# Optimization experiments

Measured on AMD Instinct MI355X. Metric: run time of the kernel, lower is better.

Reference implementation:

```python
import jax, jax.numpy as jnp
import numpy as np
import math

B, S, D, H_HEADS, K_SPAN = 2, 2048, 64, 12, 512  # batch, seq, head dim, heads, pos_ebd_size


def setup_inputs() -> dict:
    key = jax.random.key(0)
    ks = jax.random.split(key, 12)
    init = lambda k, shp: (jax.random.normal(k, shp, dtype=jnp.float32) * 0.02)
    H = jax.random.normal(ks[0], (B, S, D), dtype=jnp.float32)
    pos_embeddings = jax.random.normal(ks[1], (2 * K_SPAN, D), dtype=jnp.float32)
    # classic DeBERTa relative positions: i - j (2-D, as required by the torch code path)
    idx = jnp.arange(S)
    relative_pos = (idx[:, None] - idx[None, :]).astype(jnp.int64)
    OH = H_HEADS * D
    return {
        "H": H,
        "pos_embeddings": pos_embeddings,
        "relative_pos": relative_pos,
        "Wq": init(ks[2], (OH, D)), "bq": jnp.zeros((OH,), jnp.float32),
        "Wk": init(ks[3], (OH, D)), "bk": jnp.zeros((OH,), jnp.float32),
        "Wv": init(ks[4], (OH, D)), "bv": jnp.zeros((OH,), jnp.float32),
        "Wpq": init(ks[5], (OH, D)), "bpq": jnp.zeros((OH,), jnp.float32),
        "Wpk": init(ks[6], (OH, D)), "bpk": jnp.zeros((OH,), jnp.float32),
    }


def _heads(x):
    # [..., S, h*d] -> [..., h, S, d]
    b, s, _ = x.shape
    return x.reshape(b, s, H_HEADS, D).transpose(0, 2, 1, 3)


def reference(H, pos_embeddings, relative_pos, Wq, bq, Wk, bk, Wv, bv, Wpq, bpq, Wpk, bpk):
    proj = lambda x, W, b: x @ W.T + b
    q = _heads(proj(H, Wq, bq))  # [B,h,S,d]
    k = _heads(proj(H, Wk, bk))
    v = _heads(proj(H, Wv, bv))

    # content-to-content scores
    scores = jnp.einsum('bhqd,bhkd->bhqk', q, k)  # [B,h,S,S]

    # relative position projections over the full 2K span
    pk = proj(pos_embeddings, Wpk, bpk).reshape(2 * K_SPAN, H_HEADS, D).transpose(1, 0, 2)  # [h,2K,d]
    pq = proj(pos_embeddings, Wpq, bpq).reshape(2 * K_SPAN, H_HEADS, D).transpose(1, 0, 2)

    rel = relative_pos.astype(jnp.int32)
    # content-to-position: gather over 2K axis with clamped (i-j)+K
    c2p = jnp.einsum('bhqd,hrd->bhqr', q, pk)  # [B,h,S,2K]
    c2p_pos = jnp.clip(rel + K_SPAN, 0, 2 * K_SPAN - 1)  # [S,S]
    c2p_idx = jnp.broadcast_to(c2p_pos[None, None], (B, H_HEADS, S, S))
    c2p_att = jnp.take_along_axis(c2p, c2p_idx, axis=-1)  # [B,h,S,S]

    # position-to-content: gather over 2K axis with clamped -(i-j)+K, then transpose
    p2c = jnp.einsum('bhkd,hrd->bhkr', k, pq)  # [B,h,S,2K]
    p2c_pos = jnp.clip(-rel + K_SPAN, 0, 2 * K_SPAN - 1)
    p2c_idx = jnp.broadcast_to(p2c_pos[None, None], (B, H_HEADS, S, S))
    p2c_att = jnp.take_along_axis(p2c, p2c_idx, axis=-1).swapaxes(-1, -2)  # [B,h,S,S]

    scores = (scores + c2p_att + p2c_att) / math.sqrt(D * 3)
    probs = jax.nn.softmax(scores, axis=-1)
    ctx = jnp.einsum('bhqk,bhkd->bhqd', probs, v)  # [B,h,S,d]
    return ctx.transpose(0, 2, 1, 3).reshape(B, S, H_HEADS * D)
```

## Files before the change

### kernel.cpp

```cpp
#include <hip/hip_runtime.h>
#include <math.h>


#define S_LEN 2048
#define NH    12
#define TWOK  1024
#define QSZ   3145728
#define PSZ   786432
#define POSF  11010048

typedef __bf16 bf16x8 __attribute__((ext_vector_type(8)));
typedef unsigned short u16x8 __attribute__((ext_vector_type(8)));
typedef float f32x4  __attribute__((ext_vector_type(4)));
typedef float f32x16 __attribute__((ext_vector_type(16)));
typedef unsigned int u32x2 __attribute__((ext_vector_type(2)));
typedef unsigned int u32x4 __attribute__((ext_vector_type(4)));

__device__ __forceinline__ unsigned short f2bf(float f) {
  return __builtin_bit_cast(unsigned short, (__bf16)f);
}
__device__ __forceinline__ unsigned pk2bf(float a, float b) {
  return ((unsigned)__builtin_bit_cast(unsigned short, (__bf16)b) << 16)
       | (unsigned)__builtin_bit_cast(unsigned short, (__bf16)a);
}
__device__ __forceinline__ float bf2f(unsigned short h) {
  return __builtin_bit_cast(float, ((unsigned)h) << 16);
}
__device__ __forceinline__ bf16x8 ld_bf8(const unsigned short* p) {
  return __builtin_bit_cast(bf16x8, *(const u16x8*)p);
}

__global__ __launch_bounds__(256) void prep_kernel(
    const float* __restrict__ Hx, const float* __restrict__ pos,
    const float* __restrict__ Wq, const float* __restrict__ Wk,
    const float* __restrict__ Wv, const float* __restrict__ Wpk,
    const float* __restrict__ Wpq,
    const float* __restrict__ bq, const float* __restrict__ bk,
    const float* __restrict__ bv, const float* __restrict__ bpk,
    const float* __restrict__ bpq,
    unsigned short* __restrict__ whi, unsigned short* __restrict__ wlo,
    unsigned short* __restrict__ wall, float* __restrict__ ball) {
  int idx = blockIdx.x * 256 + threadIdx.x;
  if (idx < 327680) {
    float v = (idx < 262144) ? Hx[idx] : pos[idx - 262144];
    __bf16 hi = (__bf16)v;
    float lo = v - (float)hi;
    whi[idx] = __builtin_bit_cast(unsigned short, hi);
    wlo[idx] = f2bf(lo);
  } else if (idx < 573440) {
    int k = idx - 327680;
    int mat = k / 49152, off = k - mat * 49152;
    const float* W = mat==0?Wq: mat==1?Wk: mat==2?Wv: mat==3?Wpk:Wpq;
    wall[k] = f2bf(W[off]);
  } else if (idx < 577280) {
    int k = idx - 573440;
    int mat = k / 768, off = k - mat * 768;
    const float* B = mat==0?bq: mat==1?bk: mat==2?bv: mat==3?bpk:bpq;
    ball[k] = B[off];
  }
}

__global__ __launch_bounds__(256) void proj_gemm(
    const unsigned short* __restrict__ whi, const unsigned short* __restrict__ wlo,
    const unsigned short* __restrict__ wall, const float* __restrict__ ball,
    unsigned short* __restrict__ ws) {
  unsigned short* qg  = ws;
  unsigned short* kg  = ws + QSZ;
  unsigned short* vtg = ws + 2 * QSZ;
  unsigned short* pkg = ws + 3 * QSZ;
  unsigned short* pqg = ws + 3 * QSZ + PSZ;

  int bid = blockIdx.x;
  int rbase, obase, wrow, isA;
  if (bid < 2304) { rbase = (bid / 36) * 64;        obase = (bid % 36) * 64; wrow = obase;        isA = 1; }
  else { int b2 = bid - 2304; rbase = 4096 + (b2 / 24) * 64; obase = (b2 % 24) * 64; wrow = 2304 + obase; isA = 0; }

  int tid = threadIdx.x, w = tid >> 6, l = tid & 63, lg = l >> 4, lr = l & 15;
  int xrow = rbase + w * 16 + lr;

  bf16x8 ah[2], al[2];
  #pragma unroll
  for (int ks = 0; ks < 2; ++ks) {
    ah[ks] = ld_bf8(whi + xrow * 64 + ks * 32 + 8 * lg);
    al[ks] = ld_bf8(wlo + xrow * 64 + ks * 32 + 8 * lg);
  }

  int mat = obase / 768;
  int h = ((obase % 768) >> 6);

  #pragma unroll
  for (int jb = 0; jb < 4; ++jb) {
    f32x4 acc = {0.f, 0.f, 0.f, 0.f};
    #pragma unroll
    for (int ks = 0; ks < 2; ++ks) {
      bf16x8 bfrag = ld_bf8(wall + (wrow + jb * 16 + lr) * 64 + ks * 32 + 8 * lg);
      acc = __builtin_amdgcn_mfma_f32_16x16x32_bf16(ah[ks], bfrag, acc, 0, 0, 0);
      acc = __builtin_amdgcn_mfma_f32_16x16x32_bf16(al[ks], bfrag, acc, 0, 0, 0);
    }
    float bias = ball[wrow + jb * 16 + lr];
    int d = jb * 16 + lr;
    #pragma unroll
    for (int r = 0; r < 4; ++r) {
      int orow = rbase + w * 16 + 4 * lg + r;
      unsigned short val = f2bf(acc[r] + bias);
      if (isA) {
        int bb = orow >> 11, i = orow & 2047, bh = bb * NH + h;
        if (mat == 0)      qg[(bh * S_LEN + i) * 64 + d] = val;
        else if (mat == 1) kg[(bh * S_LEN + i) * 64 + d] = val;
        else               vtg[(bh * 64 + d) * S_LEN + i] = val;
      } else {
        int prow = orow - 4096;
        if (mat == 0) pkg[(h * TWOK + prow) * 64 + d] = val;
        else          pqg[(h * TWOK + prow) * 64 + d] = val;
      }
    }
  }
}

__global__ __launch_bounds__(256) void pos_dots(
    const unsigned short* __restrict__ ws, float* __restrict__ c2p0,
    float* __restrict__ c2p1023, float* __restrict__ p2c0,
    float* __restrict__ p2c1023) {
  int t = blockIdx.x * 256 + threadIdx.x;
  int isK = t >= 49152;
  int row = isK ? t - 49152 : t;
  int h = (row >> 11) % NH;
  const unsigned short* src = ws + (isK ? QSZ : 0) + row * 64;
  const unsigned short* pA = ws + 3 * QSZ + (isK ? PSZ : 0) + (h * TWOK) * 64;
  const unsigned short* pB = pA + 1023 * 64;
  float a0 = 0.f, a1 = 0.f;
  #pragma unroll
  for (int c = 0; c < 8; ++c) {
    u16x8 xv = *(const u16x8*)(src + c * 8);
    u16x8 av = *(const u16x8*)(pA + c * 8);
    u16x8 bv = *(const u16x8*)(pB + c * 8);
    #pragma unroll
    for (int e = 0; e < 8; ++e) {
      float x = bf2f(xv[e]);
      a0 += x * bf2f(av[e]);
      a1 += x * bf2f(bv[e]);
    }
  }
  if (isK) { p2c0[row] = a0; p2c1023[row] = a1; }
  else     { c2p0[row] = a0; c2p1023[row] = a1; }
}

__global__ __launch_bounds__(128, 2) void attn_kernel(
    const unsigned short* __restrict__ ws, float* __restrict__ out) {
  const unsigned short* qg  = ws;
  const unsigned short* kg  = ws + QSZ;
  const unsigned short* vtg = ws + 2 * QSZ;
  const unsigned short* pkg = ws + 3 * QSZ;
  const unsigned short* pqg = ws + 3 * QSZ + PSZ;
  const float* c2p0g    = (const float*)(ws + POSF);
  const float* c2p1023g = c2p0g + 49152;
  const float* p2c0g    = c2p0g + 98304;
  const float* p2c1023g = c2p0g + 147456;

  __shared__ __align__(16) unsigned short tblC[2 * 32 * 128];
  __shared__ __align__(16) unsigned short tblP[2 * 64 * 128];

  const int bid = blockIdx.x;
  const int bh = bid >> 5, itile = bid & 31;
  const int b = bh / NH, h = bh - b * NH;
  const int tid = threadIdx.x;
  const int w = tid >> 6, l = tid & 63;
  const int iL = l & 31, h5 = l >> 5;
  const int i0w = itile * 64 + w * 32;
  const int ig = i0w + iL;

  const unsigned short* qb  = qg  + bh * (S_LEN * 64);
  const unsigned short* kb  = kg  + bh * (S_LEN * 64);
  const unsigned short* vb  = vtg + bh * (64 * S_LEN);
  const unsigned short* pkb = pkg + h * (TWOK * 64);
  const unsigned short* pqb = pqg + h * (TWOK * 64);

  const float CS = 1.4426950408889634f / sqrtf(192.0f);

  bf16x8 qf[4];
  #pragma unroll
  for (int kc = 0; kc < 4; ++kc)
    qf[kc] = ld_bf8(qb + ig * 64 + kc * 16 + 8 * h5);

  const float c2pLO = c2p0g[bh * S_LEN + ig];
  const float c2pHI = c2p1023g[bh * S_LEN + ig];

  f32x16 ctx0 = 0.f, ctx1 = 0.f;
  float m_ = -1e30f, l_ = 0.f;

  char* cbase = (char*)tblC + w * 8192 + iL * 256;
  char* tPw   = (char*)tblP + w * 16384;
  char* pb0   = tPw + iL * 256;
  char* pb1   = tPw + (32 + iL) * 256;
  const int cxor = (iL & 15) << 4;

  for (int jt = 0; jt < 32; ++jt) {
    const int j0 = jt * 64;
    const int rlo = 512 + i0w - j0 - 63;
    const int rhi = rlo + 94;

    bf16x8 kf0[4], kf1[4];
    #pragma unroll
    for (int kc = 0; kc < 4; ++kc) {
      kf0[kc] = ld_bf8(kb + (j0 + iL) * 64 + kc * 16 + 8 * h5);
      kf1[kc] = ld_bf8(kb + (j0 + 32 + iL) * 64 + kc * 16 + 8 * h5);
    }
    f32x16 s0 = 0.f, s1 = 0.f;
    #pragma unroll
    for (int kc = 0; kc < 4; ++kc) {
      s0 = __builtin_amdgcn_mfma_f32_32x32x16_bf16(kf0[kc], qf[kc], s0, 0, 0, 0);
      s1 = __builtin_amdgcn_mfma_f32_32x32x16_bf16(kf1[kc], qf[kc], s1, 0, 0, 0);
    }

    if (rlo >= 1023) {
      float pa = p2c1023g[bh * S_LEN + j0 + iL];
      float pb = p2c1023g[bh * S_LEN + j0 + 32 + iL];
      #pragma unroll
      for (int r = 0; r < 16; ++r) {
        const int j32 = (r & 3) + 8 * (r >> 2) + 4 * h5;
        s0[r] = (s0[r] + c2pHI + __shfl(pa, j32)) * CS;
        s1[r] = (s1[r] + c2pHI + __shfl(pb, j32)) * CS;
      }
    } else if (rhi <= 0) {
      float pa = p2c0g[bh * S_LEN + j0 + iL];
      float pb = p2c0g[bh * S_LEN + j0 + 32 + iL];
      #pragma unroll
      for (int r = 0; r < 16; ++r) {
        const int j32 = (r & 3) + 8 * (r >> 2) + 4 * h5;
        s0[r] = (s0[r] + c2pLO + __shfl(pa, j32)) * CS;
        s1[r] = (s1[r] + c2pLO + __shfl(pb, j32)) * CS;
      }
    } else {
      const int rminc = rlo < 0 ? 0 : rlo;
      const int rmaxc = rhi > 1023 ? 1023 : rhi;
      const int bstart = rminc > 928 ? 928 : rminc;
      const int nbh = (rmaxc - bstart) >> 5;
      const int interior = (rlo >= 0) & (rhi <= 1023);
      int c_lo = (rminc - bstart) >> 5;
      int p0_lo, p1_hi;
      if (interior) {
        p0_lo = (rlo + 32 - bstart) >> 5;
        p1_hi = (rhi - 32 - bstart) >> 5;
      } else { p0_lo = c_lo; p1_hi = nbh; }

      for (int nb = c_lo; nb <= nbh; ++nb) {
        const int rrow = bstart + nb * 32 + iL;
        const int doP0 = nb >= p0_lo, doP1 = nb <= p1_hi;
        f32x16 ac = 0.f, a0 = 0.f, a1 = 0.f;
        #pragma unroll
        for (int kc = 0; kc < 4; ++kc) {
          bf16x8 fk = ld_bf8(pkb + rrow * 64 + kc * 16 + 8 * h5);
          ac = __builtin_amdgcn_mfma_f32_32x32x16_bf16(fk, qf[kc], ac, 0, 0, 0);
        }
        if (doP0 | doP1) {
          #pragma unroll
          for (int kc = 0; kc < 4; ++kc) {
            bf16x8 fq = ld_bf8(pqb + rrow * 64 + kc * 16 + 8 * h5);
            if (doP0) a0 = __builtin_amdgcn_mfma_f32_32x32x16_bf16(fq, kf0[kc], a0, 0, 0, 0);
            if (doP1) a1 = __builtin_amdgcn_mfma_f32_32x32x16_bf16(fq, kf1[kc], a1, 0, 0, 0);
          }
        }
        #pragma unroll
        for (int q4 = 0; q4 < 4; ++q4) {
          const int off = ((nb * 32 + 8 * q4 + 4 * h5) * 2) ^ cxor;
          u32x2 vc; vc[0] = pk2bf(ac[4*q4+0], ac[4*q4+1]); vc[1] = pk2bf(ac[4*q4+2], ac[4*q4+3]);
          *(u32x2*)(cbase + off) = vc;
          if (doP0) {
            u32x2 v0; v0[0] = pk2bf(a0[4*q4+0], a0[4*q4+1]); v0[1] = pk2bf(a0[4*q4+2], a0[4*q4+3]);
            *(u32x2*)(pb0 + off) = v0;
          }
          if (doP1) {
            u32x2 v1; v1[0] = pk2bf(a1[4*q4+0], a1[4*q4+1]); v1[1] = pk2bf(a1[4*q4+2], a1[4*q4+3]);
            *(u32x2*)(pb1 + off) = v1;
          }
        }
      }
      asm volatile("s_waitcnt lgkmcnt(0)" ::: "memory");

      const int D0 = ig + 512 - j0;
      if (interior) {
        const int t0 = (D0 - bstart) * 2;
        #pragma unroll
        for (int r = 0; r < 16; ++r) {
          const int j32 = (r & 3) + 8 * (r >> 2) + 4 * h5;
          const int pxr = (j32 & 15) << 4;
          const int o0 = t0 - 2 * j32, o1 = o0 - 64;
          float c0v = bf2f(*(const unsigned short*)(cbase + (o0 ^ cxor)));
          float p0v = bf2f(*(const unsigned short*)(tPw + j32 * 256 + (o0 ^ pxr)));
          float c1v = bf2f(*(const unsigned short*)(cbase + (o1 ^ cxor)));
          float p1v = bf2f(*(const unsigned short*)(tPw + (32 + j32) * 256 + (o1 ^ pxr)));
          s0[r] = (s0[r] + c0v + p0v) * CS;
          s1[r] = (s1[r] + c1v + p1v) * CS;
        }
      } else {
        #pragma unroll
        for (int r = 0; r < 16; ++r) {
          const int j32 = (r & 3) + 8 * (r >> 2) + 4 * h5;
          const int pxr = (j32 & 15) << 4;
          int rel0 = D0 - j32;       rel0 = rel0 < 0 ? 0 : (rel0 > 1023 ? 1023 : rel0);
          int rel1 = D0 - 32 - j32;  rel1 = rel1 < 0 ? 0 : (rel1 > 1023 ? 1023 : rel1);
          const int o0 = (rel0 - bstart) * 2, o1 = (rel1 - bstart) * 2;
          float c0v = bf2f(*(const unsigned short*)(cbase + (o0 ^ cxor)));
          float p0v = bf2f(*(const unsigned short*)(tPw + j32 * 256 + (o0 ^ pxr)));
          float c1v = bf2f(*(const unsigned short*)(cbase + (o1 ^ cxor)));
          float p1v = bf2f(*(const unsigned short*)(tPw + (32 + j32) * 256 + (o1 ^ pxr)));
          s0[r] = (s0[r] + c0v + p0v) * CS;
          s1[r] = (s1[r] + c1v + p1v) * CS;
        }
      }
    }

    float vmax = s0[0];
    #pragma unroll
    for (int r = 1; r < 16; ++r) vmax = fmaxf(vmax, s0[r]);
    #pragma unroll
    for (int r = 0; r < 16; ++r) vmax = fmaxf(vmax, s1[r]);
    vmax = fmaxf(vmax, __shfl_xor(vmax, 32));
    float mx = fmaxf(m_, vmax);
    float fs = __builtin_amdgcn_exp2f(m_ - mx);
    m_ = mx;
    float sum = 0.f;
    #pragma unroll
    for (int r = 0; r < 16; ++r) { s0[r] = __builtin_amdgcn_exp2f(s0[r] - mx); sum += s0[r]; }
    #pragma unroll
    for (int r = 0; r < 16; ++r) { s1[r] = __builtin_amdgcn_exp2f(s1[r] - mx); sum += s1[r]; }
    sum += __shfl_xor(sum, 32);
    l_ = l_ * fs + sum;
    if (!__all(fs == 1.0f)) { ctx0 *= fs; ctx1 *= fs; }

    bf16x8 pf[4];
    #pragma unroll
    for (int kc = 0; kc < 4; ++kc) {
      const int c = kc & 1;
      const f32x16& sj = (kc >> 1) ? s1 : s0;
      unsigned X0 = pk2bf(sj[8*c+0], sj[8*c+1]);
      unsigned X1 = pk2bf(sj[8*c+2], sj[8*c+3]);
      unsigned Y0 = pk2bf(sj[8*c+4], sj[8*c+5]);
      unsigned Y1 = pk2bf(sj[8*c+6], sj[8*c+7]);
      unsigned sx0 = (unsigned)__shfl_xor((int)X0, 32);
      unsigned sx1 = (unsigned)__shfl_xor((int)X1, 32);
      unsigned sy0 = (unsigned)__shfl_xor((int)Y0, 32);
      unsigned sy1 = (unsigned)__shfl_xor((int)Y1, 32);
      u32x4 f;
      f[0] = h5 ? sy0 : X0;
      f[1] = h5 ? sy1 : X1;
      f[2] = h5 ? Y0 : sx0;
      f[3] = h5 ? Y1 : sx1;
      pf[kc] = __builtin_bit_cast(bf16x8, f);
    }

    #pragma unroll
    for (int kc = 0; kc < 4; ++kc) {
      bf16x8 v0 = ld_bf8(vb + (iL) * S_LEN + j0 + kc * 16 + 8 * h5);
      bf16x8 v1 = ld_bf8(vb + (32 + iL) * S_LEN + j0 + kc * 16 + 8 * h5);
      ctx0 = __builtin_amdgcn_mfma_f32_32x32x16_bf16(v0, pf[kc], ctx0, 0, 0, 0);
      ctx1 = __builtin_amdgcn_mfma_f32_32x32x16_bf16(v1, pf[kc], ctx1, 0, 0, 0);
    }
  }

  float inv = 1.0f / l_;
  float* ob = out + (b * S_LEN + ig) * 768 + h * 64;
  #pragma unroll
  for (int q4 = 0; q4 < 4; ++q4) {
    float4 o0 = {ctx0[4*q4+0]*inv, ctx0[4*q4+1]*inv, ctx0[4*q4+2]*inv, ctx0[4*q4+3]*inv};
    *(float4*)(ob + 8 * q4 + 4 * h5) = o0;
    float4 o1 = {ctx1[4*q4+0]*inv, ctx1[4*q4+1]*inv, ctx1[4*q4+2]*inv, ctx1[4*q4+3]*inv};
    *(float4*)(ob + 32 + 8 * q4 + 4 * h5) = o1;
  }
}

extern "C" void kernel_launch(void* const* d_in, const int* in_sizes, int n_in,
                              void* d_out, int out_size, void* d_ws, size_t ws_size,
                              hipStream_t stream) {
  (void)in_sizes; (void)n_in; (void)out_size; (void)ws_size;
  const float* Hx  = (const float*)d_in[0];
  const float* pos = (const float*)d_in[1];
  const float* Wq  = (const float*)d_in[3];  const float* bq  = (const float*)d_in[4];
  const float* Wk  = (const float*)d_in[5];  const float* bk  = (const float*)d_in[6];
  const float* Wv  = (const float*)d_in[7];  const float* bv  = (const float*)d_in[8];
  const float* Wpq = (const float*)d_in[9];  const float* bpq = (const float*)d_in[10];
  const float* Wpk = (const float*)d_in[11]; const float* bpk = (const float*)d_in[12];
  unsigned short* ws = (unsigned short*)d_ws;

  unsigned short* scratch = (unsigned short*)d_out;
  unsigned short* whi  = scratch;
  unsigned short* wlo  = scratch + 327680;
  unsigned short* wall = scratch + 655360;
  float*          ball = (float*)(scratch + 901120);

  float* c2p0g    = (float*)(ws + POSF);
  float* c2p1023g = c2p0g + 49152;
  float* p2c0g    = c2p0g + 98304;
  float* p2c1023g = c2p0g + 147456;

  prep_kernel<<<2255, 256, 0, stream>>>(Hx, pos, Wq, Wk, Wv, Wpk, Wpq,
                                        bq, bk, bv, bpk, bpq, whi, wlo, wall, ball);
  proj_gemm<<<2688, 256, 0, stream>>>(whi, wlo, wall, ball, ws);
  pos_dots<<<384, 256, 0, stream>>>(ws, c2p0g, c2p1023g, p2c0g, p2c1023g);
  attn_kernel<<<768, 128, 0, stream>>>(ws, (float*)d_out);
}
```

Measured before the change: 345.5 us.

## Split attention into single-wave blocks, remap grid, hoist V loads, relayout c2p table

The attention kernel now runs one 64-thread wave per block instead of two, with a 1536-block grid. Block indices are remapped so that consecutive blocks cover different batch-head pairs. V fragments are loaded at the start of each key tile so their latency overlaps the score computation. The c2p shared table changes from swizzled rows per query to a column-major [rel][i] layout with scalar bf16 stores and loads. Smaller blocks should raise occupancy and improve scheduling and L2 locality, at the cost of more live registers for the V fragments and more, narrower LDS stores.

Result: faster. 334.4 us (-3.2%).

```diff
diff --git a/kernel.cpp b/kernel.cpp
--- a/kernel.cpp
+++ b/kernel.cpp
@@ -145,7 +145,7 @@
   else     { c2p0[row] = a0; c2p1023[row] = a1; }
 }
 
-__global__ __launch_bounds__(128, 2) void attn_kernel(
+__global__ __launch_bounds__(64, 2) void attn_kernel(
     const unsigned short* __restrict__ ws, float* __restrict__ out) {
   const unsigned short* qg  = ws;
   const unsigned short* kg  = ws + QSZ;
@@ -157,16 +157,17 @@
   const float* p2c0g    = c2p0g + 98304;
   const float* p2c1023g = c2p0g + 147456;
 
-  __shared__ __align__(16) unsigned short tblC[2 * 32 * 128];
-  __shared__ __align__(16) unsigned short tblP[2 * 64 * 128];
+  __shared__ __align__(16) unsigned short tblC[96 * 32];
+  __shared__ __align__(16) unsigned short tblP[64 * 128];
 
   const int bid = blockIdx.x;
-  const int bh = bid >> 5, itile = bid & 31;
+  const int g = bid & 7, r = bid >> 3;
+  const int bh = 8 * (r % 3) + g;
+  const int it32 = r / 3;
   const int b = bh / NH, h = bh - b * NH;
-  const int tid = threadIdx.x;
-  const int w = tid >> 6, l = tid & 63;
+  const int l = threadIdx.x & 63;
   const int iL = l & 31, h5 = l >> 5;
-  const int i0w = itile * 64 + w * 32;
+  const int i0w = it32 * 32;
   const int ig = i0w + iL;
 
   const unsigned short* qb  = qg  + bh * (S_LEN * 64);
@@ -188,11 +189,10 @@
   f32x16 ctx0 = 0.f, ctx1 = 0.f;
   float m_ = -1e30f, l_ = 0.f;
 
-  char* cbase = (char*)tblC + w * 8192 + iL * 256;
-  char* tPw   = (char*)tblP + w * 16384;
-  char* pb0   = tPw + iL * 256;
-  char* pb1   = tPw + (32 + iL) * 256;
-  const int cxor = (iL & 15) << 4;
+  char* tPw = (char*)tblP;
+  char* pb0 = tPw + iL * 256;
+  char* pb1 = tPw + (32 + iL) * 256;
+  const int wxor = (iL & 15) << 4;
 
   for (int jt = 0; jt < 32; ++jt) {
     const int j0 = jt * 64;
@@ -205,6 +205,13 @@
       kf0[kc] = ld_bf8(kb + (j0 + iL) * 64 + kc * 16 + 8 * h5);
       kf1[kc] = ld_bf8(kb + (j0 + 32 + iL) * 64 + kc * 16 + 8 * h5);
     }
+    bf16x8 vf0[4], vf1[4];
+    #pragma unroll
+    for (int kc = 0; kc < 4; ++kc) {
+      vf0[kc] = ld_bf8(vb + (iL) * S_LEN + j0 + kc * 16 + 8 * h5);
+      vf1[kc] = ld_bf8(vb + (32 + iL) * S_LEN + j0 + kc * 16 + 8 * h5);
+    }
+
     f32x16 s0 = 0.f, s1 = 0.f;
     #pragma unroll
     for (int kc = 0; kc < 4; ++kc) {
@@ -262,9 +269,14 @@
         }
         #pragma unroll
         for (int q4 = 0; q4 < 4; ++q4) {
-          const int off = ((nb * 32 + 8 * q4 + 4 * h5) * 2) ^ cxor;
-          u32x2 vc; vc[0] = pk2bf(ac[4*q4+0], ac[4*q4+1]); vc[1] = pk2bf(ac[4*q4+2], ac[4*q4+3]);
-          *(u32x2*)(cbase + off) = vc;
+          const int Rq = nb * 32 + 8 * q4 + 4 * h5;
+          #pragma unroll
+          for (int e = 0; e < 4; ++e)
+            tblC[(Rq + e) * 32 + iL] = f2bf(ac[4 * q4 + e]);
+        }
+        #pragma unroll
+        for (int q4 = 0; q4 < 4; ++q4) {
+          const int off = ((nb * 32 + 8 * q4 + 4 * h5) * 2) ^ wxor;
           if (doP0) {
             u32x2 v0; v0[0] = pk2bf(a0[4*q4+0], a0[4*q4+1]); v0[1] = pk2bf(a0[4*q4+2], a0[4*q4+3]);
             *(u32x2*)(pb0 + off) = v0;
@@ -279,15 +291,15 @@
 
       const int D0 = ig + 512 - j0;
       if (interior) {
-        const int t0 = (D0 - bstart) * 2;
+        const int rb0 = D0 - bstart;
         #pragma unroll
         for (int r = 0; r < 16; ++r) {
           const int j32 = (r & 3) + 8 * (r >> 2) + 4 * h5;
           const int pxr = (j32 & 15) << 4;
-          const int o0 = t0 - 2 * j32, o1 = o0 - 64;
-          float c0v = bf2f(*(const unsigned short*)(cbase + (o0 ^ cxor)));
+          const int o0 = (rb0 - j32) * 2, o1 = o0 - 64;
+          float c0v = bf2f(tblC[(rb0 - j32) * 32 + iL]);
+          float c1v = bf2f(tblC[(rb0 - 32 - j32) * 32 + iL]);
           float p0v = bf2f(*(const unsigned short*)(tPw + j32 * 256 + (o0 ^ pxr)));
-          float c1v = bf2f(*(const unsigned short*)(cbase + (o1 ^ cxor)));
           float p1v = bf2f(*(const unsigned short*)(tPw + (32 + j32) * 256 + (o1 ^ pxr)));
           s0[r] = (s0[r] + c0v + p0v) * CS;
           s1[r] = (s1[r] + c1v + p1v) * CS;
@@ -299,11 +311,11 @@
           const int pxr = (j32 & 15) << 4;
           int rel0 = D0 - j32;       rel0 = rel0 < 0 ? 0 : (rel0 > 1023 ? 1023 : rel0);
           int rel1 = D0 - 32 - j32;  rel1 = rel1 < 0 ? 0 : (rel1 > 1023 ? 1023 : rel1);
-          const int o0 = (rel0 - bstart) * 2, o1 = (rel1 - bstart) * 2;
-          float c0v = bf2f(*(const unsigned short*)(cbase + (o0 ^ cxor)));
-          float p0v = bf2f(*(const unsigned short*)(tPw + j32 * 256 + (o0 ^ pxr)));
-          float c1v = bf2f(*(const unsigned short*)(cbase + (o1 ^ cxor)));
-          float p1v = bf2f(*(const unsigned short*)(tPw + (32 + j32) * 256 + (o1 ^ pxr)));
+          const int rb0 = rel0 - bstart, rb1 = rel1 - bstart;
+          float c0v = bf2f(tblC[rb0 * 32 + iL]);
+          float c1v = bf2f(tblC[rb1 * 32 + iL]);
+          float p0v = bf2f(*(const unsigned short*)(tPw + j32 * 256 + ((rb0 * 2) ^ pxr)));
+          float p1v = bf2f(*(const unsigned short*)(tPw + (32 + j32) * 256 + ((rb1 * 2) ^ pxr)));
           s0[r] = (s0[r] + c0v + p0v) * CS;
           s1[r] = (s1[r] + c1v + p1v) * CS;
         }
@@ -351,10 +363,8 @@
 
     #pragma unroll
     for (int kc = 0; kc < 4; ++kc) {
-      bf16x8 v0 = ld_bf8(vb + (iL) * S_LEN + j0 + kc * 16 + 8 * h5);
-      bf16x8 v1 = ld_bf8(vb + (32 + iL) * S_LEN + j0 + kc * 16 + 8 * h5);
-      ctx0 = __builtin_amdgcn_mfma_f32_32x32x16_bf16(v0, pf[kc], ctx0, 0, 0, 0);
-      ctx1 = __builtin_amdgcn_mfma_f32_32x32x16_bf16(v1, pf[kc], ctx1, 0, 0, 0);
+      ctx0 = __builtin_amdgcn_mfma_f32_32x32x16_bf16(vf0[kc], pf[kc], ctx0, 0, 0, 0);
+      ctx1 = __builtin_amdgcn_mfma_f32_32x32x16_bf16(vf1[kc], pf[kc], ctx1, 0, 0, 0);
     }
   }
 
@@ -397,5 +407,5 @@
                                         bq, bk, bv, bpk, bpq, whi, wlo, wall, ball);
   proj_gemm<<<2688, 256, 0, stream>>>(whi, wlo, wall, ball, ws);
   pos_dots<<<384, 256, 0, stream>>>(ws, c2p0g, c2p1023g, p2c0g, p2c1023g);
-  attn_kernel<<<768, 128, 0, stream>>>(ws, (float*)d_out);
-}
+  attn_kernel<<<1536, 64, 0, stream>>>(ws, (float*)d_out);
+}
```
